# Optimization experiments

Measured on AMD Instinct MI355X. Metric: run time of the kernel, lower is better.

The kernel has to match this reference:

```python
import jax, jax.numpy as jnp
import numpy as np
import math

NB_STEPS = 50  # matches init kwarg nb_steps


def cc_quadrature(nb_steps):
    # Clenshaw-Curtis weights/nodes, identical to UMNN's compute_cc_weights.
    lam = np.arange(nb_steps + 1, dtype=np.float64).reshape(-1, 1)
    lam = np.cos((lam @ lam.T) * math.pi / nb_steps)
    lam[:, 0] = 0.5
    lam[:, -1] = 0.5 * lam[:, -1]
    lam = lam * 2.0 / nb_steps
    W = np.arange(nb_steps + 1, dtype=np.float64).reshape(-1, 1)
    W[np.arange(1, nb_steps + 1, 2)] = 0
    W = 2.0 / (1.0 - W ** 2)
    W[0] = 1
    W[np.arange(1, nb_steps + 1, 2)] = 0
    cc_weights = (lam.T @ W).astype(np.float32)                 # [K, 1]
    steps = np.cos(np.arange(nb_steps + 1, dtype=np.float64).reshape(-1, 1)
                   * math.pi / nb_steps).astype(np.float32)     # [K, 1]
    return jnp.asarray(cc_weights), jnp.asarray(steps)


def integrand_mlp(xh, W1, b1, W2, b2, W3, b3, W4, b4):
    y = jax.nn.relu(jnp.einsum('bkd,hd->bkh', xh, W1) + b1)
    y = jax.nn.relu(jnp.einsum('bkh,gh->bkg', y, W2) + b2)
    y = jax.nn.relu(jnp.einsum('bkg,fg->bkf', y, W3) + b3)
    y = jnp.einsum('bkf,of->bko', y, W4) + b4
    return jax.nn.elu(y) + 1.0


def setup_inputs() -> dict:
    key = jax.random.key(0)
    ks = jax.random.split(key, 10)
    B, HD, IN_D = 16384, 128, 64
    x = jax.random.normal(ks[0], (B, 1), dtype=jnp.float32)
    h = jax.random.normal(ks[1], (B, IN_D - 1), dtype=jnp.float32)
    def lin(k, fan_out, fan_in):
        return jax.random.normal(k, (fan_out, fan_in), dtype=jnp.float32) / np.sqrt(fan_in)
    return {
        'x': x, 'h': h,
        'W1': lin(ks[2], HD, IN_D), 'b1': jax.random.normal(ks[3], (HD,), dtype=jnp.float32) * 0.01,
        'W2': lin(ks[4], HD, HD),   'b2': jax.random.normal(ks[5], (HD,), dtype=jnp.float32) * 0.01,
        'W3': lin(ks[6], HD, HD),   'b3': jax.random.normal(ks[7], (HD,), dtype=jnp.float32) * 0.01,
        'W4': lin(ks[8], 1, HD),    'b4': jax.random.normal(ks[9], (1,), dtype=jnp.float32) * 0.01,
    }


def reference(x, h, W1, b1, W2, b2, W3, b3, W4, b4):
    cc_w, steps = cc_quadrature(NB_STEPS)          # [K,1], [K,1]
    xmax = jnp.max(x) + 10.0
    x0 = x                                          # [B,1]
    xT = jnp.zeros_like(x) + xmax                   # xfinal broadcast
    # quadrature points X_steps: [B, K, 1]
    X = x0[:, None, :] + (xT - x0)[:, None, :] * (steps[None, :, :] + 1.0) * 0.5
    B, K = X.shape[0], X.shape[1]
    hK = jnp.broadcast_to(h[:, None, :], (B, K, h.shape[1]))
    xh = jnp.concatenate([X, hK], axis=-1)          # [B, K, in_d]
    f = integrand_mlp(xh, W1, b1, W2, b2, W3, b3, W4, b4)  # [B, K, 1]
    z = jnp.sum(f * cc_w[None, :, :], axis=1)       # [B, 1]
    return z * (xT - x0) * 0.5
```

## Files before the change

kernel.cpp:

```cpp
#include <hip/hip_runtime.h>
#include <hip/hip_bf16.h>
#include <math.h>


#define B_N    16384
#define KQ     51
#define HD     128
#define IND    64
#define BLK    128
#define GRID   1024
#define RPB    16
#define SPB    (RPB * KQ)
#define TPB2   (SPB / 16)
#define HPITCH 20

typedef __attribute__((ext_vector_type(8))) short short8;
typedef __attribute__((ext_vector_type(4))) float f32x4;

union S8U { short8 s8; unsigned u[4]; };

__device__ __forceinline__ unsigned short f2bf(float f) {
    __hip_bfloat16 t = __float2bfloat16(f);
    return *reinterpret_cast<unsigned short*>(&t);
}

#if defined(__gfx950__) && defined(__has_builtin)
#if __has_builtin(__builtin_amdgcn_cvt_pk_bf16_f32)
#define HAVE_PK_BF16 1
#endif
#endif

__device__ __forceinline__ unsigned pk_bf16(float lo, float hi) {
#ifdef HAVE_PK_BF16
    typedef __attribute__((ext_vector_type(2))) __bf16 bfv2;
    bfv2 r = __builtin_amdgcn_cvt_pk_bf16_f32(lo, hi);
    return *reinterpret_cast<unsigned*>(&r);
#else
    return (unsigned)f2bf(lo) | ((unsigned)f2bf(hi) << 16);
#endif
}

__launch_bounds__(BLK, 2)
__global__ void umnn_fused(const float* __restrict__ x,  const float* __restrict__ h,
                           const float* __restrict__ W1, const float* __restrict__ b1,
                           const float* __restrict__ W2, const float* __restrict__ b2,
                           const float* __restrict__ W3, const float* __restrict__ b3,
                           const float* __restrict__ W4, const float* __restrict__ b4,
                           float* __restrict__ out)
{
    __shared__ __align__(16) float hpL[RPB * HD];
    __shared__ __align__(16) char  y2b[2][16 * 256];
    __shared__ __align__(16) float hshT[63 * HPITCH];
    __shared__ float vs[2][SPB];
    __shared__ float xL[RPB];
    __shared__ float sSteps[KQ], sCcw[KQ];
    __shared__ float red2[2];

    const int tid  = threadIdx.x;
    const int w    = tid >> 6;
    const int lane = tid & 63;
    const int q    = lane >> 4;
    const int lm   = lane & 15;
    const int swz  = lm & 7;
    const int rowBase = blockIdx.x * RPB;

    if (tid < KQ) {
        const int j = tid;
        const float pi50 = 0.06283185307179586f;
        sSteps[j] = __cosf((float)j * pi50);
        float s = 0.0f;
        for (int i = 0; i <= 50; i += 2) {
            float Wi = (i == 0) ? 1.0f : 2.0f / (1.0f - (float)(i * i));
            float lam;
            if (j == 0) lam = 0.5f;
            else {
                int mp = (i * j) % 100;
                lam = __cosf((float)mp * pi50);
                if (j == 50) lam *= 0.5f;
            }
            s += (lam * 0.04f) * Wi;
        }
        sCcw[j] = s;
    }
    {
        const f32x4* x4 = (const f32x4*)x;
        float mx = -1e30f;
        for (int i = tid; i < B_N / 4; i += BLK) {
            f32x4 v = x4[i];
            mx = fmaxf(fmaxf(mx, fmaxf(v[0], v[1])), fmaxf(v[2], v[3]));
        }
        #pragma unroll
        for (int d = 32; d > 0; d >>= 1) mx = fmaxf(mx, __shfl_xor(mx, d));
        if (lane == 0) red2[w] = mx;
    }
    for (int i = tid; i < RPB * 63; i += BLK) {
        int r = i / 63, d = i - r * 63;
        hshT[d * HPITCH + r] = h[rowBase * 63 + i];
    }
    if (tid < RPB) xL[tid] = x[rowBase + tid];
    __syncthreads();

    const float xmax = fmaxf(red2[0], red2[1]) + 10.0f;

    {
        const int n = tid;
        float acc[RPB];
        const float b1v = b1[n];
        #pragma unroll
        for (int r = 0; r < RPB; ++r) acc[r] = b1v;
        const float* wr = W1 + n * IND + 1;
        #pragma unroll 1
        for (int d = 0; d < IND - 1; ++d) {
            float wv = wr[d];
            const float* ht = hshT + d * HPITCH;
            #pragma unroll
            for (int rc = 0; rc < RPB / 4; ++rc) {
                f32x4 hv = *(const f32x4*)(ht + rc * 4);
                acc[rc * 4 + 0] = fmaf(wv, hv[0], acc[rc * 4 + 0]);
                acc[rc * 4 + 1] = fmaf(wv, hv[1], acc[rc * 4 + 1]);
                acc[rc * 4 + 2] = fmaf(wv, hv[2], acc[rc * 4 + 2]);
                acc[rc * 4 + 3] = fmaf(wv, hv[3], acc[rc * 4 + 3]);
            }
        }
        #pragma unroll
        for (int r = 0; r < RPB; ++r) hpL[r * HD + n] = acc[r];
    }

    float w1x[32];
    #pragma unroll
    for (int kk = 0; kk < 4; ++kk)
        #pragma unroll
        for (int j = 0; j < 8; ++j)
            w1x[kk * 8 + j] = W1[(kk * 32 + q * 8 + j) * IND];

    short8 W2A[4][4], W3A[4][4];
    f32x4  b2c[4], b3c[4], W4c[4];
    #pragma unroll
    for (int nt = 0; nt < 4; ++nt) {
        const int ntg = w * 4 + nt;
        #pragma unroll
        for (int kk = 0; kk < 4; ++kk) {
            const float* p2 = W2 + (ntg * 16 + lm) * HD + kk * 32 + q * 8;
            const float* p3 = W3 + (ntg * 16 + lm) * HD + kk * 32 + q * 8;
            S8U a2, a3;
            #pragma unroll
            for (int j = 0; j < 4; ++j) {
                a2.u[j] = pk_bf16(p2[2 * j], p2[2 * j + 1]);
                a3.u[j] = pk_bf16(p3[2 * j], p3[2 * j + 1]);
            }
            W2A[nt][kk] = a2.s8; W3A[nt][kk] = a3.s8;
        }
        b2c[nt] = *(const f32x4*)(b2 + ntg * 16 + q * 4);
        b3c[nt] = *(const f32x4*)(b3 + ntg * 16 + q * 4);
        W4c[nt] = *(const f32x4*)(W4 + ntg * 16 + q * 4);
    }
    const float b4v = b4[0];
    float* vsW = vs[w];
    __syncthreads();

    const int S0 = blockIdx.x * SPB;

    #pragma unroll 1
    for (int tt = 0; tt < TPB2; ++tt) {
        char* buf = y2b[tt & 1];

        const int s   = S0 + tt * 16 + lm;
        const unsigned row = (unsigned)s / KQ;
        const int k   = s - (int)row * KQ;
        const int rl  = (int)row - rowBase;
        const float x0 = xL[rl];
        const float X  = fmaf((xmax - x0) * 0.5f, sSteps[k] + 1.0f, x0);
        short8 Y1[4];
        #pragma unroll
        for (int kk = 0; kk < 4; ++kk) {
            const float* hp = hpL + rl * HD + kk * 32 + q * 8;
            f32x4 ha = *(const f32x4*)hp;
            f32x4 hb = *(const f32x4*)(hp + 4);
            S8U u;
            u.u[0] = pk_bf16(fmaxf(fmaf(X, w1x[kk*8+0], ha[0]), 0.f),
                             fmaxf(fmaf(X, w1x[kk*8+1], ha[1]), 0.f));
            u.u[1] = pk_bf16(fmaxf(fmaf(X, w1x[kk*8+2], ha[2]), 0.f),
                             fmaxf(fmaf(X, w1x[kk*8+3], ha[3]), 0.f));
            u.u[2] = pk_bf16(fmaxf(fmaf(X, w1x[kk*8+4], hb[0]), 0.f),
                             fmaxf(fmaf(X, w1x[kk*8+5], hb[1]), 0.f));
            u.u[3] = pk_bf16(fmaxf(fmaf(X, w1x[kk*8+6], hb[2]), 0.f),
                             fmaxf(fmaf(X, w1x[kk*8+7], hb[3]), 0.f));
            Y1[kk] = u.s8;
        }

        f32x4 C[4];
        #pragma unroll
        for (int nt = 0; nt < 4; ++nt) C[nt] = b2c[nt];
        #pragma unroll
        for (int kk = 0; kk < 4; ++kk)
            #pragma unroll
            for (int nt = 0; nt < 4; ++nt)
                C[nt] = __builtin_amdgcn_mfma_f32_16x16x32_bf16(W2A[nt][kk], Y1[kk], C[nt], 0, 0, 0);

        #pragma unroll
        for (int nt = 0; nt < 4; ++nt) {
            const int cch = 2 * (w * 4 + nt) + (q >> 1);
            unsigned lo = pk_bf16(fmaxf(C[nt][0], 0.f), fmaxf(C[nt][1], 0.f));
            unsigned hi = pk_bf16(fmaxf(C[nt][2], 0.f), fmaxf(C[nt][3], 0.f));
            *(int2*)(buf + lm * 256 + ((cch ^ swz) << 4) + ((q & 1) << 3))
                = make_int2((int)lo, (int)hi);
        }
        __syncthreads();

        short8 Y2[4];
        #pragma unroll
        for (int kk = 0; kk < 4; ++kk)
            Y2[kk] = *(const short8*)(buf + lm * 256 + (((kk * 4 + q) ^ swz) << 4));
        #pragma unroll
        for (int nt = 0; nt < 4; ++nt) C[nt] = b3c[nt];
        #pragma unroll
        for (int kk = 0; kk < 4; ++kk)
            #pragma unroll
            for (int nt = 0; nt < 4; ++nt)
                C[nt] = __builtin_amdgcn_mfma_f32_16x16x32_bf16(W3A[nt][kk], Y2[kk], C[nt], 0, 0, 0);

        float p = 0.f;
        #pragma unroll
        for (int nt = 0; nt < 4; ++nt) {
            p = fmaf(fmaxf(C[nt][0], 0.f), W4c[nt][0], p);
            p = fmaf(fmaxf(C[nt][1], 0.f), W4c[nt][1], p);
            p = fmaf(fmaxf(C[nt][2], 0.f), W4c[nt][2], p);
            p = fmaf(fmaxf(C[nt][3], 0.f), W4c[nt][3], p);
        }
        p += __shfl_xor(p, 16);
        p += __shfl_xor(p, 32);
        if (lane < 16) vsW[tt * 16 + lm] = p;
    }
    __syncthreads();

    if (w == 0) {
        const int r   = lane >> 2;
        const int sub = lane & 3;
        float a = 0.f;
        #pragma unroll 1
        for (int j = 0; j < 13; ++j) {
            int k = sub + 4 * j;
            if (k < KQ) {
                int sl = r * KQ + k;
                float y4 = vs[0][sl] + vs[1][sl] + b4v;
                float f  = (y4 > 0.f) ? (y4 + 1.f) : __expf(y4);
                a = fmaf(f, sCcw[k], a);
            }
        }
        a += __shfl_xor(a, 1);
        a += __shfl_xor(a, 2);
        if (sub == 0)
            out[rowBase + r] = a * (xmax - xL[r]) * 0.5f;
    }
}

extern "C" void kernel_launch(void* const* d_in, const int* in_sizes, int n_in,
                              void* d_out, int out_size, void* d_ws, size_t ws_size,
                              hipStream_t stream)
{
    const float* x  = (const float*)d_in[0];
    const float* h  = (const float*)d_in[1];
    const float* W1 = (const float*)d_in[2];
    const float* b1 = (const float*)d_in[3];
    const float* W2 = (const float*)d_in[4];
    const float* b2 = (const float*)d_in[5];
    const float* W3 = (const float*)d_in[6];
    const float* b3 = (const float*)d_in[7];
    const float* W4 = (const float*)d_in[8];
    const float* b4 = (const float*)d_in[9];
    float* out = (float*)d_out;

    umnn_fused<<<GRID, BLK, 0, stream>>>(x, h, W1, b1, W2, b2, W3, b3,
                                         W4, b4, out);
}
```

Measured before the change: 190.1 us.

## Halve rows per block, double grid, and raise occupancy to four blocks per SM

Cuts rows per block from 16 to 8 and doubles the grid, so each block processes 26 padded 16-sample tiles, with samples past the last row clamped and discarded. The h-projection transpose buffer and the per-wave output buffer now share one LDS region, which shrinks LDS so that launch bounds can ask for 4 blocks per CU. Swizzled LDS offsets are precomputed outside the loop. The goal is more resident waves to hide latency, paid for with padded tile work (416 vs 408 samples), duplicated per-block weight setup, and a tighter register budget that could cause spills.

After: 661.8 us. 3.48x slower.

```diff
diff --git a/kernel.cpp b/kernel.cpp
--- a/kernel.cpp
+++ b/kernel.cpp
@@ -8,11 +8,11 @@
 #define HD     128
 #define IND    64
 #define BLK    128
-#define GRID   1024
-#define RPB    16
+#define GRID   2048
+#define RPB    8
 #define SPB    (RPB * KQ)
-#define TPB2   (SPB / 16)
-#define HPITCH 20
+#define NT16   26
+#define HPITCH 12
 
 typedef __attribute__((ext_vector_type(8))) short short8;
 typedef __attribute__((ext_vector_type(4))) float f32x4;
@@ -40,7 +40,7 @@
 #endif
 }
 
-__launch_bounds__(BLK, 2)
+__launch_bounds__(BLK, 4)
 __global__ void umnn_fused(const float* __restrict__ x,  const float* __restrict__ h,
                            const float* __restrict__ W1, const float* __restrict__ b1,
                            const float* __restrict__ W2, const float* __restrict__ b2,
@@ -49,12 +49,14 @@
                            float* __restrict__ out)
 {
     __shared__ __align__(16) float hpL[RPB * HD];
-    __shared__ __align__(16) char  y2b[2][16 * 256];
-    __shared__ __align__(16) float hshT[63 * HPITCH];
-    __shared__ float vs[2][SPB];
+    __shared__ __align__(16) char  y2b[2 * 4096];
+    __shared__ __align__(16) float uSh[2 * SPB];
     __shared__ float xL[RPB];
     __shared__ float sSteps[KQ], sCcw[KQ];
     __shared__ float red2[2];
+
+    float* hshT = uSh;
+    float (*vs)[SPB] = (float(*)[SPB])uSh;
 
     const int tid  = threadIdx.x;
     const int w    = tid >> 6;
@@ -155,25 +157,31 @@
         W4c[nt] = *(const f32x4*)(W4 + ntg * 16 + q * 4);
     }
     const float b4v = b4[0];
-    float* vsW = vs[w];
+
+    int wOff[4], rOff[4];
+    #pragma unroll
+    for (int nt = 0; nt < 4; ++nt) {
+        const int cch = 2 * (w * 4 + nt) + (q >> 1);
+        wOff[nt] = lm * 256 + ((cch ^ swz) << 4) + ((q & 1) << 3);
+        rOff[nt] = lm * 256 + (((nt * 4 + q) ^ swz) << 4);
+    }
     __syncthreads();
 
-    const int S0 = blockIdx.x * SPB;
-
     #pragma unroll 1
-    for (int tt = 0; tt < TPB2; ++tt) {
-        char* buf = y2b[tt & 1];
-
-        const int s   = S0 + tt * 16 + lm;
-        const unsigned row = (unsigned)s / KQ;
-        const int k   = s - (int)row * KQ;
-        const int rl  = (int)row - rowBase;
-        const float x0 = xL[rl];
+    for (int tt = 0; tt < NT16; ++tt) {
+        char* buf = y2b + ((tt & 1) << 12);
+
+        const int slocal = tt * 16 + lm;
+        const int rl  = (int)((unsigned)slocal / KQ);
+        const int k   = slocal - rl * KQ;
+        const int rlc = (rl < RPB) ? rl : RPB - 1;
+        const float x0 = xL[rlc];
         const float X  = fmaf((xmax - x0) * 0.5f, sSteps[k] + 1.0f, x0);
+
         short8 Y1[4];
         #pragma unroll
         for (int kk = 0; kk < 4; ++kk) {
-            const float* hp = hpL + rl * HD + kk * 32 + q * 8;
+            const float* hp = hpL + rlc * HD + kk * 32 + q * 8;
             f32x4 ha = *(const f32x4*)hp;
             f32x4 hb = *(const f32x4*)(hp + 4);
             S8U u;
@@ -199,18 +207,16 @@
 
         #pragma unroll
         for (int nt = 0; nt < 4; ++nt) {
-            const int cch = 2 * (w * 4 + nt) + (q >> 1);
             unsigned lo = pk_bf16(fmaxf(C[nt][0], 0.f), fmaxf(C[nt][1], 0.f));
             unsigned hi = pk_bf16(fmaxf(C[nt][2], 0.f), fmaxf(C[nt][3], 0.f));
-            *(int2*)(buf + lm * 256 + ((cch ^ swz) << 4) + ((q & 1) << 3))
-                = make_int2((int)lo, (int)hi);
+            *(int2*)(buf + wOff[nt]) = make_int2((int)lo, (int)hi);
         }
         __syncthreads();
 
         short8 Y2[4];
         #pragma unroll
         for (int kk = 0; kk < 4; ++kk)
-            Y2[kk] = *(const short8*)(buf + lm * 256 + (((kk * 4 + q) ^ swz) << 4));
+            Y2[kk] = *(const short8*)(buf + rOff[kk]);
         #pragma unroll
         for (int nt = 0; nt < 4; ++nt) C[nt] = b3c[nt];
         #pragma unroll
@@ -229,28 +235,30 @@
         }
         p += __shfl_xor(p, 16);
         p += __shfl_xor(p, 32);
-        if (lane < 16) vsW[tt * 16 + lm] = p;
+        if (lane < 16 && rl < RPB) vs[w][slocal] = p;
     }
     __syncthreads();
 
     if (w == 0) {
         const int r   = lane >> 2;
         const int sub = lane & 3;
-        float a = 0.f;
-        #pragma unroll 1
-        for (int j = 0; j < 13; ++j) {
-            int k = sub + 4 * j;
-            if (k < KQ) {
-                int sl = r * KQ + k;
-                float y4 = vs[0][sl] + vs[1][sl] + b4v;
-                float f  = (y4 > 0.f) ? (y4 + 1.f) : __expf(y4);
-                a = fmaf(f, sCcw[k], a);
-            }
-        }
-        a += __shfl_xor(a, 1);
-        a += __shfl_xor(a, 2);
-        if (sub == 0)
-            out[rowBase + r] = a * (xmax - xL[r]) * 0.5f;
+        if (r < RPB) {
+            float a = 0.f;
+            #pragma unroll 1
+            for (int j = 0; j < 13; ++j) {
+                int kq = sub + 4 * j;
+                if (kq < KQ) {
+                    int sl = r * KQ + kq;
+                    float y4 = vs[0][sl] + vs[1][sl] + b4v;
+                    float f  = (y4 > 0.f) ? (y4 + 1.f) : __expf(y4);
+                    a = fmaf(f, sCcw[kq], a);
+                }
+            }
+            a += __shfl_xor(a, 1);
+            a += __shfl_xor(a, 2);
+            if (sub == 0)
+                out[rowBase + r] = a * (xmax - xL[r]) * 0.5f;
+        }
     }
 }
 
```
